# Kernel tuning notes

Hardware: AMD Instinct MI355X
Metric: run time of the kernel (lower is better)

The kernel has to match this reference:

```python
import jax, jax.numpy as jnp
import numpy as np

N_NODES = 100000
N_EDGES = 1600000
IN_C, HID_C, OUT_C = 128, 128, 64


def setup_inputs() -> dict:
    key = jax.random.key(0)
    ks = jax.random.split(key, 8)
    x = jax.random.normal(ks[0], (N_NODES, IN_C), dtype=jnp.float32)
    edge_index = jax.random.randint(ks[1], (2, N_EDGES), 0, N_NODES, dtype=jnp.int64)
    # SAGEConv params: lin_l (aggregated neighbors, with bias), lin_r (root, no bias)
    s1 = 1.0 / np.sqrt(IN_C)
    s2 = 1.0 / np.sqrt(HID_C)
    W1_l = jax.random.uniform(ks[2], (IN_C, HID_C), jnp.float32, -s1, s1)
    b1_l = jnp.zeros((HID_C,), jnp.float32)
    W1_r = jax.random.uniform(ks[3], (IN_C, HID_C), jnp.float32, -s1, s1)
    W2_l = jax.random.uniform(ks[4], (HID_C, OUT_C), jnp.float32, -s2, s2)
    b2_l = jnp.zeros((OUT_C,), jnp.float32)
    W2_r = jax.random.uniform(ks[5], (HID_C, OUT_C), jnp.float32, -s2, s2)
    return {"x": x, "edge_index": edge_index, "W1_l": W1_l, "b1_l": b1_l,
            "W1_r": W1_r, "W2_l": W2_l, "b2_l": b2_l, "W2_r": W2_r}


def _sage_conv(x, src, dst, W_l, b_l, W_r):
    # gather source features, scatter-max reduce onto destinations
    msg = x[src]                                             # [E, C]
    aggr = jax.ops.segment_max(msg, dst, num_segments=N_NODES)
    aggr = jnp.where(jnp.isfinite(aggr), aggr, 0.0)          # isolated nodes -> 0 (PyG behavior)
    return aggr @ W_l + b_l + x @ W_r


def reference(x, edge_index, W1_l, b1_l, W1_r, W2_l, b2_l, W2_r):
    src, dst = edge_index[0], edge_index[1]
    h = _sage_conv(x, src, dst, W1_l, b1_l, W1_r)
    h = jax.nn.relu(h)
    # dropout is identity in eval mode
    out = _sage_conv(h, src, dst, W2_l, b2_l, W2_r)
    return out
```

## Files before the change

### kernel.cpp

```cpp
#include <hip/hip_runtime.h>
#include <cstdint>

#define NNODES 100000
#define NEDGES 1600000
#define NBKT   196
#define CAP    9216
#define BIN_CHUNK 4096
#define GBIN ((NEDGES + BIN_CHUNK - 1) / BIN_CHUNK)
#define GCVT (NNODES * 16 / 256)
#define GWPK 24

typedef __attribute__((ext_vector_type(8))) __bf16 bf16x8;
typedef __attribute__((ext_vector_type(4))) float f32x4;
typedef short v2s __attribute__((ext_vector_type(2)));

__device__ __forceinline__ unsigned short f2bf_rne(float f) {
    unsigned int u = __float_as_uint(f);
    u += 0x7fffu + ((u >> 16) & 1u);
    return (unsigned short)(u >> 16);
}
__device__ __forceinline__ unsigned encdec(unsigned u) {
    return u ^ (((u & 0x80008000u) >> 15) * 0x7FFFu);
}
__device__ __forceinline__ unsigned pkmax(unsigned a, unsigned b) {
    v2s r = __builtin_elementwise_max(__builtin_bit_cast(v2s, a), __builtin_bit_cast(v2s, b));
    return __builtin_bit_cast(unsigned, r);
}
__device__ __forceinline__ uint4 pkmax4(uint4 a, uint4 b) {
    uint4 r;
    r.x = pkmax(a.x, b.x); r.y = pkmax(a.y, b.y);
    r.z = pkmax(a.z, b.z); r.w = pkmax(a.w, b.w);
    return r;
}


__global__ __launch_bounds__(256) void prep_kernel(
        const int* __restrict__ src, const int* __restrict__ dst,
        unsigned int* __restrict__ binArr, int* __restrict__ bucketFill,
        const float4* __restrict__ xin, uint4* __restrict__ xeout,
        const float* __restrict__ W1l, const float* __restrict__ W1r,
        const float* __restrict__ W2l, const float* __restrict__ W2r,
        uint4* __restrict__ Wf1, uint4* __restrict__ Wf2, int nE) {
    if (blockIdx.x >= GBIN + GCVT) {
        int t = (blockIdx.x - GBIN - GCVT) * 256 + threadIdx.x;
        unsigned short s[8];
        if (t < 4096) {
            int h = t >> 11, kt = (t >> 9) & 3, nt = (t >> 6) & 7, lane = t & 63;
            const float* W = h ? W1r : W1l;
            int k0 = kt * 32 + (lane >> 4) * 8;
            int col = nt * 16 + (lane & 15);
#pragma unroll
            for (int jj = 0; jj < 8; ++jj) s[jj] = f2bf_rne(W[(k0 + jj) * 128 + col]);
            uint4 o;
            o.x = (unsigned)s[0] | ((unsigned)s[1] << 16);
            o.y = (unsigned)s[2] | ((unsigned)s[3] << 16);
            o.z = (unsigned)s[4] | ((unsigned)s[5] << 16);
            o.w = (unsigned)s[6] | ((unsigned)s[7] << 16);
            Wf1[t] = o;
        } else {
            int u = t - 4096;
            int h = u >> 10, kt = (u >> 8) & 3, nt = (u >> 6) & 3, lane = u & 63;
            const float* W = h ? W2r : W2l;
            int k0 = kt * 32 + (lane >> 4) * 8;
            int col = nt * 16 + (lane & 15);
#pragma unroll
            for (int jj = 0; jj < 8; ++jj) s[jj] = f2bf_rne(W[(k0 + jj) * 64 + col]);
            uint4 o;
            o.x = (unsigned)s[0] | ((unsigned)s[1] << 16);
            o.y = (unsigned)s[2] | ((unsigned)s[3] << 16);
            o.z = (unsigned)s[4] | ((unsigned)s[5] << 16);
            o.w = (unsigned)s[6] | ((unsigned)s[7] << 16);
            Wf2[u] = o;
        }
        return;
    }
    if (blockIdx.x >= GBIN) {
        int t = (blockIdx.x - GBIN) * 256 + threadIdx.x;
        int s = t / (NNODES * 8);
        int rem = t - s * (NNODES * 8);
        int n = rem >> 3, j = rem & 7;
        int f = n * 32 + s * 16 + j * 2;
        float4 v0 = xin[f], v1 = xin[f + 1];
        uint4 o;
        o.x = encdec((unsigned)f2bf_rne(v0.x) | ((unsigned)f2bf_rne(v0.y) << 16));
        o.y = encdec((unsigned)f2bf_rne(v0.z) | ((unsigned)f2bf_rne(v0.w) << 16));
        o.z = encdec((unsigned)f2bf_rne(v1.x) | ((unsigned)f2bf_rne(v1.y) << 16));
        o.w = encdec((unsigned)f2bf_rne(v1.z) | ((unsigned)f2bf_rne(v1.w) << 16));
        xeout[t] = o;
        return;
    }
    __shared__ unsigned int stage[BIN_CHUNK];
    __shared__ unsigned char bof[BIN_CHUNK];
    __shared__ int cnt[256], cstart[256], cfill[256], gbase[256];
    const int tid = threadIdx.x;
    const int blockStart = blockIdx.x * BIN_CHUNK;
    const int chunkN = min(BIN_CHUNK, nE - blockStart);
    cnt[tid] = 0;
    __syncthreads();
    int myd[16], mys[16];
#pragma unroll
    for (int i = 0; i < 16; ++i) {
        int idx = i * 256 + tid;
        if (idx < chunkN) {
            myd[i] = dst[blockStart + idx];
            mys[i] = src[blockStart + idx];
            atomicAdd(&cnt[myd[i] >> 9], 1);
        }
    }
    __syncthreads();
    int v = cnt[tid];
    for (int off = 1; off < 256; off <<= 1) {
        int add = (tid >= off) ? cnt[tid - off] : 0;
        __syncthreads();
        cnt[tid] += add;
        __syncthreads();
    }
    cstart[tid] = cnt[tid] - v;
    cfill[tid] = cnt[tid] - v;
    if (tid < NBKT && v > 0) gbase[tid] = atomicAdd(&bucketFill[tid], v);
    __syncthreads();
#pragma unroll
    for (int i = 0; i < 16; ++i) {
        int idx = i * 256 + tid;
        if (idx < chunkN) {
            int b = myd[i] >> 9;
            int p = atomicAdd(&cfill[b], 1);
            stage[p] = ((unsigned)(myd[i] & 511) << 17) | (unsigned)mys[i];
            bof[p] = (unsigned char)b;
        }
    }
    __syncthreads();
#pragma unroll
    for (int i = 0; i < 16; ++i) {
        int idx = i * 256 + tid;
        if (idx < chunkN) {
            int b = bof[idx];
            int slot = gbase[b] + (idx - cstart[b]);
            if (slot < CAP) binArr[(size_t)b * CAP + slot] = stage[idx];
        }
    }
}

__global__ __launch_bounds__(512) void build_csr_kernel(
        const unsigned int* __restrict__ binArr, const int* __restrict__ bucketFill,
        unsigned int* __restrict__ sortedSrc,
        int* __restrict__ rowBeg, int* __restrict__ rowEnd) {
    __shared__ unsigned int stage[CAP];
    __shared__ int ncnt[512], nstart[512];
    const int b = blockIdx.x;
    const int t = threadIdx.x;
    const int cnt_b = min(bucketFill[b], CAP);
    ncnt[t] = 0;
    __syncthreads();
    for (int i = t; i < cnt_b; i += 512) {
        unsigned int e = binArr[(size_t)b * CAP + i];
        stage[i] = e;
        atomicAdd(&ncnt[e >> 17], 1);
    }
    __syncthreads();
    int v = ncnt[t];
    for (int off = 1; off < 512; off <<= 1) {
        int add = (t >= off) ? ncnt[t - off] : 0;
        __syncthreads();
        ncnt[t] += add;
        __syncthreads();
    }
    int start = ncnt[t] - v;
    nstart[t] = start;
    int n = (b << 9) + t;
    if (n < NNODES) {
        rowBeg[n] = b * CAP + start;
        rowEnd[n] = b * CAP + start + v;
    }
    __syncthreads();
    for (int i = t; i < cnt_b; i += 512) {
        unsigned int e = stage[i];
        int p = atomicAdd(&nstart[e >> 17], 1);
        sortedSrc[(size_t)b * CAP + p] = e & 0x1FFFFu;
    }
}

__global__ __launch_bounds__(256) void aggregate_sl2(
        const uint4* __restrict__ xsl,
        const int* __restrict__ rowBeg,
        const int* __restrict__ rowEnd,
        const unsigned int* __restrict__ sortedSrc,
        uint4* __restrict__ asl,
        int nN) {
    const int r    = blockIdx.x & 7;
    const int c    = blockIdx.x >> 3;
    const int s    = r >> 2;
    const int g    = c * 4 + (r & 3);
    if (g * 32 >= nN) return;
    const int wv   = threadIdx.x >> 6;
    const int lane = threadIdx.x & 63;
    const int k    = lane >> 3;
    const int j    = lane & 7;
    const int kb   = k << 3;
    const int n    = g * 32 + wv * 8 + k;
    const size_t srow = (size_t)s * nN;

    const int beg = rowBeg[n], end = rowEnd[n];
    const int m = end - beg;

    int maxm = m;
    maxm = max(maxm, __shfl_xor(maxm, 8));
    maxm = max(maxm, __shfl_xor(maxm, 16));
    maxm = max(maxm, __shfl_xor(maxm, 32));

    int idv0 = 0, idv1 = 0;
    if (m > 0) {
        idv0 = (int)sortedSrc[min(beg + j,     end - 1)];
        idv1 = (int)sortedSrc[min(beg + 8 + j, end - 1)];
    }
    int a0 = __shfl(idv0, kb | 0), a1 = __shfl(idv0, kb | 1);
    int a2 = __shfl(idv0, kb | 2), a3 = __shfl(idv0, kb | 3);
    int a4 = __shfl(idv0, kb | 4), a5 = __shfl(idv0, kb | 5);
    int a6 = __shfl(idv0, kb | 6), a7 = __shfl(idv0, kb | 7);
    int b0 = __shfl(idv1, kb | 0), b1 = __shfl(idv1, kb | 1);
    int b2 = __shfl(idv1, kb | 2), b3 = __shfl(idv1, kb | 3);
    int b4 = __shfl(idv1, kb | 4), b5 = __shfl(idv1, kb | 5);
    int b6 = __shfl(idv1, kb | 6), b7 = __shfl(idv1, kb | 7);
    uint4 q0 = xsl[(srow + a0) * 8 + j];
    uint4 q1 = xsl[(srow + a1) * 8 + j];
    uint4 q2 = xsl[(srow + a2) * 8 + j];
    uint4 q3 = xsl[(srow + a3) * 8 + j];
    uint4 q4 = xsl[(srow + a4) * 8 + j];
    uint4 q5 = xsl[(srow + a5) * 8 + j];
    uint4 q6 = xsl[(srow + a6) * 8 + j];
    uint4 q7 = xsl[(srow + a7) * 8 + j];
    uint4 q8  = xsl[(srow + b0) * 8 + j];
    uint4 q9  = xsl[(srow + b1) * 8 + j];
    uint4 q10 = xsl[(srow + b2) * 8 + j];
    uint4 q11 = xsl[(srow + b3) * 8 + j];
    uint4 q12 = xsl[(srow + b4) * 8 + j];
    uint4 q13 = xsl[(srow + b5) * 8 + j];
    uint4 q14 = xsl[(srow + b6) * 8 + j];
    uint4 q15 = xsl[(srow + b7) * 8 + j];
    uint4 accA = pkmax4(pkmax4(pkmax4(q0, q1), pkmax4(q2, q3)),
                        pkmax4(pkmax4(q4, q5), pkmax4(q6, q7)));
    uint4 accB = pkmax4(pkmax4(pkmax4(q8, q9), pkmax4(q10, q11)),
                        pkmax4(pkmax4(q12, q13), pkmax4(q14, q15)));
    uint4 acc = pkmax4(accA, accB);

    for (int e0 = 16; e0 < maxm; e0 += 8) {
        if (e0 < m) {
            int idt = (int)sortedSrc[min(beg + e0 + j, end - 1)];
            int t0 = __shfl(idt, kb | 0), t1 = __shfl(idt, kb | 1);
            int t2 = __shfl(idt, kb | 2), t3 = __shfl(idt, kb | 3);
            int t4 = __shfl(idt, kb | 4), t5 = __shfl(idt, kb | 5);
            int t6 = __shfl(idt, kb | 6), t7 = __shfl(idt, kb | 7);
            uint4 u0 = xsl[(srow + t0) * 8 + j];
            uint4 u1 = xsl[(srow + t1) * 8 + j];
            uint4 u2 = xsl[(srow + t2) * 8 + j];
            uint4 u3 = xsl[(srow + t3) * 8 + j];
            uint4 u4 = xsl[(srow + t4) * 8 + j];
            uint4 u5 = xsl[(srow + t5) * 8 + j];
            uint4 u6 = xsl[(srow + t6) * 8 + j];
            uint4 u7 = xsl[(srow + t7) * 8 + j];
            acc = pkmax4(acc, pkmax4(pkmax4(pkmax4(u0, u1), pkmax4(u2, u3)),
                                     pkmax4(pkmax4(u4, u5), pkmax4(u6, u7))));
        }
    }

    uint4 o;
    if (m > 0) { o = acc; }
    else       { o.x = o.y = o.z = o.w = 0u; }
    asl[(srow + n) * 8 + j] = o;
}

template<int BN, bool RELU, bool ENCOUT, typename OutT>
__global__ __launch_bounds__(256, 4) void sage_gemm_lean(
        const uint4* __restrict__ AggE,
        const uint4* __restrict__ RootE,
        const uint4* __restrict__ Wf,
        const float* __restrict__ bias,
        OutT* __restrict__ C,
        int M) {
    constexpr int NT = BN / 16;
    const int tid = threadIdx.x;
    const int w = tid >> 6;
    const int lane = tid & 63;
    const int quad = lane >> 4;
    const int mrow = lane & 15;
    const int base0 = blockIdx.x * 128 + w * 32;

    const int r0 = min(base0 + mrow, M - 1);
    const int r1 = min(base0 + 16 + mrow, M - 1);

    f32x4 acc[2][NT];
#pragma unroll
    for (int mt = 0; mt < 2; ++mt)
#pragma unroll
        for (int nt = 0; nt < NT; ++nt) acc[mt][nt] = (f32x4){0.f, 0.f, 0.f, 0.f};

#pragma unroll
    for (int kt = 0; kt < 4; ++kt) {
        const int q = kt * 4 + quad;
        const size_t sl = (size_t)(q >> 3) * M;
        const int jj = q & 7;
        uint4 ta0 = AggE[(sl + r0) * 8 + jj];
        uint4 ta1 = AggE[(sl + r1) * 8 + jj];
        uint4 tr0 = RootE[(sl + r0) * 8 + jj];
        uint4 tr1 = RootE[(sl + r1) * 8 + jj];
        ta0.x = encdec(ta0.x); ta0.y = encdec(ta0.y); ta0.z = encdec(ta0.z); ta0.w = encdec(ta0.w);
        ta1.x = encdec(ta1.x); ta1.y = encdec(ta1.y); ta1.z = encdec(ta1.z); ta1.w = encdec(ta1.w);
        tr0.x = encdec(tr0.x); tr0.y = encdec(tr0.y); tr0.z = encdec(tr0.z); tr0.w = encdec(tr0.w);
        tr1.x = encdec(tr1.x); tr1.y = encdec(tr1.y); tr1.z = encdec(tr1.z); tr1.w = encdec(tr1.w);
        bf16x8 aa0 = __builtin_bit_cast(bf16x8, ta0);
        bf16x8 aa1 = __builtin_bit_cast(bf16x8, ta1);
        bf16x8 ar0 = __builtin_bit_cast(bf16x8, tr0);
        bf16x8 ar1 = __builtin_bit_cast(bf16x8, tr1);
#pragma unroll
        for (int nt = 0; nt < NT; ++nt) {
            bf16x8 b0 = __builtin_bit_cast(bf16x8, Wf[(kt * NT + nt) * 64 + lane]);
            acc[0][nt] = __builtin_amdgcn_mfma_f32_16x16x32_bf16(aa0, b0, acc[0][nt], 0, 0, 0);
            acc[1][nt] = __builtin_amdgcn_mfma_f32_16x16x32_bf16(aa1, b0, acc[1][nt], 0, 0, 0);
            bf16x8 b1 = __builtin_bit_cast(bf16x8, Wf[((4 + kt) * NT + nt) * 64 + lane]);
            acc[0][nt] = __builtin_amdgcn_mfma_f32_16x16x32_bf16(ar0, b1, acc[0][nt], 0, 0, 0);
            acc[1][nt] = __builtin_amdgcn_mfma_f32_16x16x32_bf16(ar1, b1, acc[1][nt], 0, 0, 0);
        }
    }

#pragma unroll
    for (int mt = 0; mt < 2; ++mt) {
        const int rowD = base0 + mt * 16 + quad * 4;
#pragma unroll
        for (int nt = 0; nt < NT; ++nt) {
            int col = nt * 16 + mrow;
            float bv = bias[col];
#pragma unroll
            for (int r = 0; r < 4; ++r) {
                int grow = rowD + r;
                if (grow < M) {
                    float v = acc[mt][nt][r] + bv;
                    if (RELU) v = fmaxf(v, 0.0f);
                    if constexpr (ENCOUT) {
                        unsigned u = f2bf_rne(v);
                        u ^= ((u >> 15) & 1u) * 0x7FFFu;
                        C[((size_t)(col >> 6) * M + grow) * 64 + (col & 63)] = (OutT)u;
                    } else {
                        C[(size_t)grow * BN + col] = (OutT)v;
                    }
                }
            }
        }
    }
}

extern "C" void kernel_launch(void* const* d_in, const int* in_sizes, int n_in,
                              void* d_out, int out_size, void* d_ws, size_t ws_size,
                              hipStream_t stream) {
    const float* x   = (const float*)d_in[0];
    const int*   ei  = (const int*)d_in[1];
    const float* W1l = (const float*)d_in[2];
    const float* b1l = (const float*)d_in[3];
    const float* W1r = (const float*)d_in[4];
    const float* W2l = (const float*)d_in[5];
    const float* b2l = (const float*)d_in[6];
    const float* W2r = (const float*)d_in[7];
    float* out = (float*)d_out;

    const int* src = ei;
    const int* dst = ei + NEDGES;

    char* ws = (char*)d_ws;
    unsigned short* xe    = (unsigned short*)ws; ws += (size_t)NNODES * 128 * 2;
    unsigned short* he    = (unsigned short*)ws; ws += (size_t)NNODES * 128 * 2;
    unsigned short* aggrE = (unsigned short*)ws; ws += (size_t)NNODES * 128 * 2;
    unsigned int* binArr    = (unsigned int*)ws; ws += (size_t)NBKT * CAP * 4;
    unsigned int* sortedSrc = (unsigned int*)ws; ws += (size_t)NBKT * CAP * 4;
    int* rowBeg     = (int*)ws; ws += (size_t)NNODES * 4;
    int* rowEnd     = (int*)ws; ws += (size_t)NNODES * 4;
    int* bucketFill = (int*)ws; ws += 256 * 4;
    uint4* Wf1 = (uint4*)ws; ws += 4096 * 16;
    uint4* Wf2 = (uint4*)ws; ws += 2048 * 16;

    const int gAgg = 8 * ((NNODES / 32 + 3) / 4);
    const int gGemm = (NNODES + 127) / 128;

    hipMemsetAsync(bucketFill, 0, 256 * sizeof(int), stream);
    prep_kernel<<<GBIN + GCVT + GWPK, 256, 0, stream>>>(
        src, dst, binArr, bucketFill, (const float4*)x, (uint4*)xe,
        W1l, W1r, W2l, W2r, Wf1, Wf2, NEDGES);
    build_csr_kernel<<<NBKT, 512, 0, stream>>>(binArr, bucketFill, sortedSrc, rowBeg, rowEnd);

    aggregate_sl2<<<gAgg, 256, 0, stream>>>((const uint4*)xe, rowBeg, rowEnd, sortedSrc,
                                            (uint4*)aggrE, NNODES);
    sage_gemm_lean<128, true, true, unsigned short><<<gGemm, 256, 0, stream>>>(
        (const uint4*)aggrE, (const uint4*)xe, Wf1, b1l, he, NNODES);
    aggregate_sl2<<<gAgg, 256, 0, stream>>>((const uint4*)he, rowBeg, rowEnd, sortedSrc,
                                            (uint4*)aggrE, NNODES);
    sage_gemm_lean<64, false, false, float><<<gGemm, 256, 0, stream>>>(
        (const uint4*)aggrE, (const uint4*)he, Wf2, b2l, out, NNODES);
}
```

Before: 281.4 us.

## Fuse neighbor max-aggregation with SAGE GEMM through LDS per 16-node tile

Merges the gather/segment-max aggregation kernel and the bf16 MFMA GEMM into one kernel per layer. Each 256-thread block aggregates 16 nodes into shared memory, then four waves each compute a column slice of the output. This removes the aggregated-feature intermediate buffer and two kernel launches. In exchange each block re-reads the weight fragments for only 16 rows, and the MFMA work per wave shrinks, which may reduce GEMM efficiency and occupancy balance.

```diff
diff --git a/kernel.cpp b/kernel.cpp
--- a/kernel.cpp
+++ b/kernel.cpp
@@ -180,169 +180,144 @@
     }
 }
 
-__global__ __launch_bounds__(256) void aggregate_sl2(
+template<int BN, bool RELU, bool ENCOUT, typename OutT>
+__global__ __launch_bounds__(256) void sage_fused(
         const uint4* __restrict__ xsl,
         const int* __restrict__ rowBeg,
         const int* __restrict__ rowEnd,
         const unsigned int* __restrict__ sortedSrc,
-        uint4* __restrict__ asl,
-        int nN) {
-    const int r    = blockIdx.x & 7;
-    const int c    = blockIdx.x >> 3;
-    const int s    = r >> 2;
-    const int g    = c * 4 + (r & 3);
-    if (g * 32 >= nN) return;
-    const int wv   = threadIdx.x >> 6;
-    const int lane = threadIdx.x & 63;
-    const int k    = lane >> 3;
-    const int j    = lane & 7;
-    const int kb   = k << 3;
-    const int n    = g * 32 + wv * 8 + k;
-    const size_t srow = (size_t)s * nN;
-
-    const int beg = rowBeg[n], end = rowEnd[n];
-    const int m = end - beg;
-
-    int maxm = m;
-    maxm = max(maxm, __shfl_xor(maxm, 8));
-    maxm = max(maxm, __shfl_xor(maxm, 16));
-    maxm = max(maxm, __shfl_xor(maxm, 32));
-
-    int idv0 = 0, idv1 = 0;
-    if (m > 0) {
-        idv0 = (int)sortedSrc[min(beg + j,     end - 1)];
-        idv1 = (int)sortedSrc[min(beg + 8 + j, end - 1)];
-    }
-    int a0 = __shfl(idv0, kb | 0), a1 = __shfl(idv0, kb | 1);
-    int a2 = __shfl(idv0, kb | 2), a3 = __shfl(idv0, kb | 3);
-    int a4 = __shfl(idv0, kb | 4), a5 = __shfl(idv0, kb | 5);
-    int a6 = __shfl(idv0, kb | 6), a7 = __shfl(idv0, kb | 7);
-    int b0 = __shfl(idv1, kb | 0), b1 = __shfl(idv1, kb | 1);
-    int b2 = __shfl(idv1, kb | 2), b3 = __shfl(idv1, kb | 3);
-    int b4 = __shfl(idv1, kb | 4), b5 = __shfl(idv1, kb | 5);
-    int b6 = __shfl(idv1, kb | 6), b7 = __shfl(idv1, kb | 7);
-    uint4 q0 = xsl[(srow + a0) * 8 + j];
-    uint4 q1 = xsl[(srow + a1) * 8 + j];
-    uint4 q2 = xsl[(srow + a2) * 8 + j];
-    uint4 q3 = xsl[(srow + a3) * 8 + j];
-    uint4 q4 = xsl[(srow + a4) * 8 + j];
-    uint4 q5 = xsl[(srow + a5) * 8 + j];
-    uint4 q6 = xsl[(srow + a6) * 8 + j];
-    uint4 q7 = xsl[(srow + a7) * 8 + j];
-    uint4 q8  = xsl[(srow + b0) * 8 + j];
-    uint4 q9  = xsl[(srow + b1) * 8 + j];
-    uint4 q10 = xsl[(srow + b2) * 8 + j];
-    uint4 q11 = xsl[(srow + b3) * 8 + j];
-    uint4 q12 = xsl[(srow + b4) * 8 + j];
-    uint4 q13 = xsl[(srow + b5) * 8 + j];
-    uint4 q14 = xsl[(srow + b6) * 8 + j];
-    uint4 q15 = xsl[(srow + b7) * 8 + j];
-    uint4 accA = pkmax4(pkmax4(pkmax4(q0, q1), pkmax4(q2, q3)),
-                        pkmax4(pkmax4(q4, q5), pkmax4(q6, q7)));
-    uint4 accB = pkmax4(pkmax4(pkmax4(q8, q9), pkmax4(q10, q11)),
-                        pkmax4(pkmax4(q12, q13), pkmax4(q14, q15)));
-    uint4 acc = pkmax4(accA, accB);
-
-    for (int e0 = 16; e0 < maxm; e0 += 8) {
-        if (e0 < m) {
-            int idt = (int)sortedSrc[min(beg + e0 + j, end - 1)];
-            int t0 = __shfl(idt, kb | 0), t1 = __shfl(idt, kb | 1);
-            int t2 = __shfl(idt, kb | 2), t3 = __shfl(idt, kb | 3);
-            int t4 = __shfl(idt, kb | 4), t5 = __shfl(idt, kb | 5);
-            int t6 = __shfl(idt, kb | 6), t7 = __shfl(idt, kb | 7);
-            uint4 u0 = xsl[(srow + t0) * 8 + j];
-            uint4 u1 = xsl[(srow + t1) * 8 + j];
-            uint4 u2 = xsl[(srow + t2) * 8 + j];
-            uint4 u3 = xsl[(srow + t3) * 8 + j];
-            uint4 u4 = xsl[(srow + t4) * 8 + j];
-            uint4 u5 = xsl[(srow + t5) * 8 + j];
-            uint4 u6 = xsl[(srow + t6) * 8 + j];
-            uint4 u7 = xsl[(srow + t7) * 8 + j];
-            acc = pkmax4(acc, pkmax4(pkmax4(pkmax4(u0, u1), pkmax4(u2, u3)),
-                                     pkmax4(pkmax4(u4, u5), pkmax4(u6, u7))));
-        }
-    }
-
-    uint4 o;
-    if (m > 0) { o = acc; }
-    else       { o.x = o.y = o.z = o.w = 0u; }
-    asl[(srow + n) * 8 + j] = o;
-}
-
-template<int BN, bool RELU, bool ENCOUT, typename OutT>
-__global__ __launch_bounds__(256, 4) void sage_gemm_lean(
-        const uint4* __restrict__ AggE,
-        const uint4* __restrict__ RootE,
         const uint4* __restrict__ Wf,
         const float* __restrict__ bias,
         OutT* __restrict__ C,
-        int M) {
+        int nN) {
     constexpr int NT = BN / 16;
-    const int tid = threadIdx.x;
-    const int w = tid >> 6;
-    const int lane = tid & 63;
+    constexpr int NTW = BN / 64;
+    __shared__ uint4 lds[16][17];
+    const int wv   = threadIdx.x >> 6;
+    const int lane = threadIdx.x & 63;
+    const int n0   = blockIdx.x * 16;
+
+    {
+        const int s  = wv & 1;
+        const int nh = wv >> 1;
+        const int k  = lane >> 3;
+        const int j  = lane & 7;
+        const int kb = k << 3;
+        const int n  = n0 + nh * 8 + k;
+        const size_t srow = (size_t)s * nN;
+
+        const int beg = rowBeg[n], end = rowEnd[n];
+        const int m = end - beg;
+
+        int maxm = m;
+        maxm = max(maxm, __shfl_xor(maxm, 8));
+        maxm = max(maxm, __shfl_xor(maxm, 16));
+        maxm = max(maxm, __shfl_xor(maxm, 32));
+
+        int idv0 = 0, idv1 = 0;
+        if (m > 0) {
+            idv0 = (int)sortedSrc[min(beg + j,     end - 1)];
+            idv1 = (int)sortedSrc[min(beg + 8 + j, end - 1)];
+        }
+        int a0 = __shfl(idv0, kb | 0), a1 = __shfl(idv0, kb | 1);
+        int a2 = __shfl(idv0, kb | 2), a3 = __shfl(idv0, kb | 3);
+        int a4 = __shfl(idv0, kb | 4), a5 = __shfl(idv0, kb | 5);
+        int a6 = __shfl(idv0, kb | 6), a7 = __shfl(idv0, kb | 7);
+        int b0 = __shfl(idv1, kb | 0), b1 = __shfl(idv1, kb | 1);
+        int b2 = __shfl(idv1, kb | 2), b3 = __shfl(idv1, kb | 3);
+        int b4 = __shfl(idv1, kb | 4), b5 = __shfl(idv1, kb | 5);
+        int b6 = __shfl(idv1, kb | 6), b7 = __shfl(idv1, kb | 7);
+        uint4 q0  = xsl[(srow + a0) * 8 + j];
+        uint4 q1  = xsl[(srow + a1) * 8 + j];
+        uint4 q2  = xsl[(srow + a2) * 8 + j];
+        uint4 q3  = xsl[(srow + a3) * 8 + j];
+        uint4 q4  = xsl[(srow + a4) * 8 + j];
+        uint4 q5  = xsl[(srow + a5) * 8 + j];
+        uint4 q6  = xsl[(srow + a6) * 8 + j];
+        uint4 q7  = xsl[(srow + a7) * 8 + j];
+        uint4 q8  = xsl[(srow + b0) * 8 + j];
+        uint4 q9  = xsl[(srow + b1) * 8 + j];
+        uint4 q10 = xsl[(srow + b2) * 8 + j];
+        uint4 q11 = xsl[(srow + b3) * 8 + j];
+        uint4 q12 = xsl[(srow + b4) * 8 + j];
+        uint4 q13 = xsl[(srow + b5) * 8 + j];
+        uint4 q14 = xsl[(srow + b6) * 8 + j];
+        uint4 q15 = xsl[(srow + b7) * 8 + j];
+        uint4 accA = pkmax4(pkmax4(pkmax4(q0, q1), pkmax4(q2, q3)),
+                            pkmax4(pkmax4(q4, q5), pkmax4(q6, q7)));
+        uint4 accB = pkmax4(pkmax4(pkmax4(q8, q9), pkmax4(q10, q11)),
+                            pkmax4(pkmax4(q12, q13), pkmax4(q14, q15)));
+        uint4 acc = pkmax4(accA, accB);
+
+        for (int e0 = 16; e0 < maxm; e0 += 8) {
+            if (e0 < m) {
+                int idt = (int)sortedSrc[min(beg + e0 + j, end - 1)];
+                int t0 = __shfl(idt, kb | 0), t1 = __shfl(idt, kb | 1);
+                int t2 = __shfl(idt, kb | 2), t3 = __shfl(idt, kb | 3);
+                int t4 = __shfl(idt, kb | 4), t5 = __shfl(idt, kb | 5);
+                int t6 = __shfl(idt, kb | 6), t7 = __shfl(idt, kb | 7);
+                uint4 u0 = xsl[(srow + t0) * 8 + j];
+                uint4 u1 = xsl[(srow + t1) * 8 + j];
+                uint4 u2 = xsl[(srow + t2) * 8 + j];
+                uint4 u3 = xsl[(srow + t3) * 8 + j];
+                uint4 u4 = xsl[(srow + t4) * 8 + j];
+                uint4 u5 = xsl[(srow + t5) * 8 + j];
+                uint4 u6 = xsl[(srow + t6) * 8 + j];
+                uint4 u7 = xsl[(srow + t7) * 8 + j];
+                acc = pkmax4(acc, pkmax4(pkmax4(pkmax4(u0, u1), pkmax4(u2, u3)),
+                                         pkmax4(pkmax4(u4, u5), pkmax4(u6, u7))));
+            }
+        }
+
+        uint4 o;
+        if (m > 0) { o = acc; }
+        else       { o.x = o.y = o.z = o.w = 0u; }
+        lds[nh * 8 + k][s * 8 + j] = o;
+    }
+    __syncthreads();
+
     const int quad = lane >> 4;
     const int mrow = lane & 15;
-    const int base0 = blockIdx.x * 128 + w * 32;
-
-    const int r0 = min(base0 + mrow, M - 1);
-    const int r1 = min(base0 + 16 + mrow, M - 1);
-
-    f32x4 acc[2][NT];
-#pragma unroll
-    for (int mt = 0; mt < 2; ++mt)
-#pragma unroll
-        for (int nt = 0; nt < NT; ++nt) acc[mt][nt] = (f32x4){0.f, 0.f, 0.f, 0.f};
+    const int r    = n0 + mrow;
+
+    f32x4 acc[NTW];
+#pragma unroll
+    for (int t = 0; t < NTW; ++t) acc[t] = (f32x4){0.f, 0.f, 0.f, 0.f};
 
 #pragma unroll
     for (int kt = 0; kt < 4; ++kt) {
         const int q = kt * 4 + quad;
-        const size_t sl = (size_t)(q >> 3) * M;
-        const int jj = q & 7;
-        uint4 ta0 = AggE[(sl + r0) * 8 + jj];
-        uint4 ta1 = AggE[(sl + r1) * 8 + jj];
-        uint4 tr0 = RootE[(sl + r0) * 8 + jj];
-        uint4 tr1 = RootE[(sl + r1) * 8 + jj];
-        ta0.x = encdec(ta0.x); ta0.y = encdec(ta0.y); ta0.z = encdec(ta0.z); ta0.w = encdec(ta0.w);
-        ta1.x = encdec(ta1.x); ta1.y = encdec(ta1.y); ta1.z = encdec(ta1.z); ta1.w = encdec(ta1.w);
-        tr0.x = encdec(tr0.x); tr0.y = encdec(tr0.y); tr0.z = encdec(tr0.z); tr0.w = encdec(tr0.w);
-        tr1.x = encdec(tr1.x); tr1.y = encdec(tr1.y); tr1.z = encdec(tr1.z); tr1.w = encdec(tr1.w);
-        bf16x8 aa0 = __builtin_bit_cast(bf16x8, ta0);
-        bf16x8 aa1 = __builtin_bit_cast(bf16x8, ta1);
-        bf16x8 ar0 = __builtin_bit_cast(bf16x8, tr0);
-        bf16x8 ar1 = __builtin_bit_cast(bf16x8, tr1);
-#pragma unroll
-        for (int nt = 0; nt < NT; ++nt) {
-            bf16x8 b0 = __builtin_bit_cast(bf16x8, Wf[(kt * NT + nt) * 64 + lane]);
-            acc[0][nt] = __builtin_amdgcn_mfma_f32_16x16x32_bf16(aa0, b0, acc[0][nt], 0, 0, 0);
-            acc[1][nt] = __builtin_amdgcn_mfma_f32_16x16x32_bf16(aa1, b0, acc[1][nt], 0, 0, 0);
-            bf16x8 b1 = __builtin_bit_cast(bf16x8, Wf[((4 + kt) * NT + nt) * 64 + lane]);
-            acc[0][nt] = __builtin_amdgcn_mfma_f32_16x16x32_bf16(ar0, b1, acc[0][nt], 0, 0, 0);
-            acc[1][nt] = __builtin_amdgcn_mfma_f32_16x16x32_bf16(ar1, b1, acc[1][nt], 0, 0, 0);
-        }
-    }
-
-#pragma unroll
-    for (int mt = 0; mt < 2; ++mt) {
-        const int rowD = base0 + mt * 16 + quad * 4;
-#pragma unroll
-        for (int nt = 0; nt < NT; ++nt) {
-            int col = nt * 16 + mrow;
-            float bv = bias[col];
-#pragma unroll
-            for (int r = 0; r < 4; ++r) {
-                int grow = rowD + r;
-                if (grow < M) {
-                    float v = acc[mt][nt][r] + bv;
-                    if (RELU) v = fmaxf(v, 0.0f);
-                    if constexpr (ENCOUT) {
-                        unsigned u = f2bf_rne(v);
-                        u ^= ((u >> 15) & 1u) * 0x7FFFu;
-                        C[((size_t)(col >> 6) * M + grow) * 64 + (col & 63)] = (OutT)u;
-                    } else {
-                        C[(size_t)grow * BN + col] = (OutT)v;
-                    }
-                }
+        uint4 ta = lds[mrow][q];
+        uint4 tr = xsl[((size_t)(q >> 3) * nN + r) * 8 + (q & 7)];
+        ta.x = encdec(ta.x); ta.y = encdec(ta.y); ta.z = encdec(ta.z); ta.w = encdec(ta.w);
+        tr.x = encdec(tr.x); tr.y = encdec(tr.y); tr.z = encdec(tr.z); tr.w = encdec(tr.w);
+        bf16x8 aa = __builtin_bit_cast(bf16x8, ta);
+        bf16x8 ar = __builtin_bit_cast(bf16x8, tr);
+#pragma unroll
+        for (int t = 0; t < NTW; ++t) {
+            const int ct = wv * NTW + t;
+            bf16x8 wb0 = __builtin_bit_cast(bf16x8, Wf[(kt * NT + ct) * 64 + lane]);
+            acc[t] = __builtin_amdgcn_mfma_f32_16x16x32_bf16(aa, wb0, acc[t], 0, 0, 0);
+            bf16x8 wb1 = __builtin_bit_cast(bf16x8, Wf[((4 + kt) * NT + ct) * 64 + lane]);
+            acc[t] = __builtin_amdgcn_mfma_f32_16x16x32_bf16(ar, wb1, acc[t], 0, 0, 0);
+        }
+    }
+
+#pragma unroll
+    for (int t = 0; t < NTW; ++t) {
+        const int col = (wv * NTW + t) * 16 + mrow;
+        const float bv = bias[col];
+#pragma unroll
+        for (int rr = 0; rr < 4; ++rr) {
+            const int grow = n0 + quad * 4 + rr;
+            float v = acc[t][rr] + bv;
+            if (RELU) v = fmaxf(v, 0.0f);
+            if constexpr (ENCOUT) {
+                unsigned u = f2bf_rne(v);
+                u ^= ((u >> 15) & 1u) * 0x7FFFu;
+                C[((size_t)(col >> 6) * nN + grow) * 64 + (col & 63)] = (OutT)u;
+            } else {
+                C[(size_t)grow * BN + col] = (OutT)v;
             }
         }
     }
@@ -367,7 +342,6 @@
     char* ws = (char*)d_ws;
     unsigned short* xe    = (unsigned short*)ws; ws += (size_t)NNODES * 128 * 2;
     unsigned short* he    = (unsigned short*)ws; ws += (size_t)NNODES * 128 * 2;
-    unsigned short* aggrE = (unsigned short*)ws; ws += (size_t)NNODES * 128 * 2;
     unsigned int* binArr    = (unsigned int*)ws; ws += (size_t)NBKT * CAP * 4;
     unsigned int* sortedSrc = (unsigned int*)ws; ws += (size_t)NBKT * CAP * 4;
     int* rowBeg     = (int*)ws; ws += (size_t)NNODES * 4;
@@ -376,8 +350,7 @@
     uint4* Wf1 = (uint4*)ws; ws += 4096 * 16;
     uint4* Wf2 = (uint4*)ws; ws += 2048 * 16;
 
-    const int gAgg = 8 * ((NNODES / 32 + 3) / 4);
-    const int gGemm = (NNODES + 127) / 128;
+    const int gFus = NNODES / 16;
 
     hipMemsetAsync(bucketFill, 0, 256 * sizeof(int), stream);
     prep_kernel<<<GBIN + GCVT + GWPK, 256, 0, stream>>>(
@@ -385,12 +358,8 @@
         W1l, W1r, W2l, W2r, Wf1, Wf2, NEDGES);
     build_csr_kernel<<<NBKT, 512, 0, stream>>>(binArr, bucketFill, sortedSrc, rowBeg, rowEnd);
 
-    aggregate_sl2<<<gAgg, 256, 0, stream>>>((const uint4*)xe, rowBeg, rowEnd, sortedSrc,
-                                            (uint4*)aggrE, NNODES);
-    sage_gemm_lean<128, true, true, unsigned short><<<gGemm, 256, 0, stream>>>(
-        (const uint4*)aggrE, (const uint4*)xe, Wf1, b1l, he, NNODES);
-    aggregate_sl2<<<gAgg, 256, 0, stream>>>((const uint4*)he, rowBeg, rowEnd, sortedSrc,
-                                            (uint4*)aggrE, NNODES);
-    sage_gemm_lean<64, false, false, float><<<gGemm, 256, 0, stream>>>(
-        (const uint4*)aggrE, (const uint4*)he, Wf2, b2l, out, NNODES);
-}
+    sage_fused<128, true, true, unsigned short><<<gFus, 256, 0, stream>>>(
+        (const uint4*)xe, rowBeg, rowEnd, sortedSrc, Wf1, b1l, he, NNODES);
+    sage_fused<64, false, false, float><<<gFus, 256, 0, stream>>>(
+        (const uint4*)he, rowBeg, rowEnd, sortedSrc, Wf2, b2l, out, NNODES);
+}
```

After: 261.0 us. 7.2% less time.
